# Kernel optimization log

Measured on AMD Instinct MI355X. Metric: run time of the kernel, lower is better.

## Reference

```python
import jax, jax.numpy as jnp
import numpy as np

N_NODES = 100000
N_EDGES = 1600000
IN_F = 512
OUT_F = 128


def setup_inputs() -> dict:
    key = jax.random.key(0)
    k1, k2, k3, k4, k5 = jax.random.split(key, 5)
    x = jax.random.normal(k1, (N_NODES, IN_F), dtype=jnp.float32)
    adj_row = jnp.sort(jax.random.randint(k2, (N_EDGES,), 0, N_NODES, dtype=jnp.int32))
    adj_col = jax.random.randint(k3, (N_EDGES,), 0, N_NODES, dtype=jnp.int32)
    adj_vals = jax.random.uniform(k4, (N_EDGES,), dtype=jnp.float32)
    # Xavier-uniform init like nn.init.xavier_uniform_
    limit = float(np.sqrt(6.0 / (IN_F + OUT_F)))
    weight = jax.random.uniform(k5, (IN_F, OUT_F), minval=-limit, maxval=limit, dtype=jnp.float32)
    return {"x": x, "adj_row": adj_row, "adj_col": adj_col, "adj_vals": adj_vals, "weight": weight}


def reference(x, adj_row, adj_col, adj_vals, weight):
    # support = input @ weight  (dense GEMM; torch.spmm with dense-equivalent input)
    support = x @ weight                      # [N, OUT_F]
    # output = adj @ support, adj in COO: gather cols, scale, segment-sum by row
    msgs = adj_vals[:, None] * support[adj_col]          # [E, OUT_F]
    output = jax.ops.segment_sum(msgs, adj_row, num_segments=N_NODES)  # [N, OUT_F]
    return output
```

## Files before the change

kernel.cpp:

```cpp
#include <hip/hip_runtime.h>
#include <hip/hip_bf16.h>

typedef __bf16 bf16;
typedef __attribute__((ext_vector_type(8))) __bf16 bf16x8;
typedef __attribute__((ext_vector_type(4))) __bf16 bf16x4;
typedef __attribute__((ext_vector_type(2))) __bf16 bf16x2;
typedef __attribute__((ext_vector_type(4))) float f32x4;

#define IN_F 512
#define OUT_F 128
#define BM 64
#define BK 64
#define NKT (IN_F / BK)
#define RPW 8
#define WPB 4
#define PAGE 256
#define UNR 16

__global__ __launch_bounds__(256) void wt_convert_kernel(const float* __restrict__ w,
                                                         bf16* __restrict__ wt_frag) {
    int o = blockIdx.x * 256 + threadIdx.x;
    int e   = o & 7;
    int l   = (o >> 3) & 63;
    int nb  = (o >> 9) & 7;
    int kkt = o >> 12;
    int n = nb * 16 + (l & 15);
    int k = (kkt >> 1) * 64 + (kkt & 1) * 32 + (l >> 4) * 8 + e;
    wt_frag[o] = (bf16)w[k * OUT_F + n];
}

__global__ __launch_bounds__(256) void row_ptr_kernel(const int* __restrict__ adj_row,
                                                      int* __restrict__ row_ptr,
                                                      int n_edges, int n_nodes) {
    int e = blockIdx.x * 256 + threadIdx.x;
    if (e >= n_edges) return;
    int r1 = adj_row[e];
    int r0 = (e == 0) ? -1 : adj_row[e - 1];
    for (int r = r0 + 1; r <= r1; ++r) row_ptr[r] = e;
    if (e == n_edges - 1)
        for (int r = r1 + 1; r <= n_nodes; ++r) row_ptr[r] = n_edges;
}

__global__ __launch_bounds__(256) void gemm_kernel(const float* __restrict__ x,
                                                   const bf16* __restrict__ wt_frag,
                                                   bf16* __restrict__ support,
                                                   int n_nodes) {
    __shared__ bf16 As[2][BM * BK];

    const int tid  = threadIdx.x;
    const int lane = tid & 63;
    const int wid  = tid >> 6;
    const int row0 = blockIdx.x * BM;

    float4 av[4];

    auto load_tile = [&](int kt) {
        const int k0 = kt * BK;
        #pragma unroll
        for (int i = 0; i < 4; ++i) {
            int li = i * 256 + tid;
            int r = li >> 4, c4 = li & 15;
            int grow = row0 + r;
            float4 v = {0.f, 0.f, 0.f, 0.f};
            if (grow < n_nodes)
                v = *reinterpret_cast<const float4*>(x + (size_t)grow * IN_F + k0 + c4 * 4);
            av[i] = v;
        }
    };

    auto write_tile = [&](int buf) {
        char* Ab = (char*)As[buf];
        #pragma unroll
        for (int i = 0; i < 4; ++i) {
            int li = i * 256 + tid;
            int r = li >> 4, c4 = li & 15;
            bf16x4 b;
            b[0] = (bf16)av[i].x; b[1] = (bf16)av[i].y;
            b[2] = (bf16)av[i].z; b[3] = (bf16)av[i].w;
            *reinterpret_cast<bf16x4*>(Ab + ((r * 128 + c4 * 8) ^ ((r & 7) << 4))) = b;
        }
    };

    load_tile(0);
    write_tile(0);
    __syncthreads();

    f32x4 acc[4][2] = {};

    for (int kt = 0; kt < NKT; ++kt) {
        const int cur = kt & 1;

        bf16x8 b[2][2];
        #pragma unroll
        for (int kk = 0; kk < 2; ++kk)
            #pragma unroll
            for (int n = 0; n < 2; ++n) {
                int f = (kt * 2 + kk) * 8 + (wid * 2 + n);
                b[kk][n] = *reinterpret_cast<const bf16x8*>(wt_frag + ((size_t)f * 64 + lane) * 8);
            }

        if (kt < NKT - 1) load_tile(kt + 1);

        const char* Ab = (const char*)As[cur];
        #pragma unroll
        for (int kk = 0; kk < 2; ++kk) {
            const int kbyte = kk * 64 + (lane >> 4) * 16;
            bf16x8 a[4];
            #pragma unroll
            for (int m = 0; m < 4; ++m) {
                int r = m * 16 + (lane & 15);
                a[m] = *reinterpret_cast<const bf16x8*>(Ab + ((r * 128 + kbyte) ^ ((r & 7) << 4)));
            }
            #pragma unroll
            for (int m = 0; m < 4; ++m)
                #pragma unroll
                for (int n = 0; n < 2; ++n)
                    acc[m][n] = __builtin_amdgcn_mfma_f32_16x16x32_bf16(a[m], b[kk][n], acc[m][n], 0, 0, 0);
        }

        if (kt < NKT - 1) {
            write_tile(cur ^ 1);
            __syncthreads();
        }
    }

    #pragma unroll
    for (int m = 0; m < 4; ++m) {
        #pragma unroll
        for (int n = 0; n < 2; ++n) {
            #pragma unroll
            for (int j = 0; j < 4; ++j) {
                int gm = row0 + m * 16 + (lane >> 4) * 4 + j;
                int gn = wid * 32 + n * 16 + (lane & 15);
                if (gm < n_nodes)
                    support[(size_t)gm * OUT_F + gn] = (bf16)acc[m][n][j];
            }
        }
    }
}

__global__ __launch_bounds__(256, 8) void scatter_kernel(const int* __restrict__ adj_row,
                                                         const int* __restrict__ adj_col,
                                                         const float* __restrict__ adj_vals,
                                                         const bf16* __restrict__ support,
                                                         const int* __restrict__ row_ptr,
                                                         float* __restrict__ out,
                                                         int n_nodes) {
    __shared__ int   srow[WPB][PAGE];
    __shared__ int   scol[WPB][PAGE];
    __shared__ float sval[WPB][PAGE];

    const int t  = threadIdx.x & 63;
    const int w  = threadIdx.x >> 6;
    const int r0 = blockIdx.x * (WPB * RPW) + w * RPW;
    if (r0 >= n_nodes) return;
    const int rEnd = min(r0 + RPW, n_nodes);
    const int eLo  = row_ptr[r0];
    const int eHi  = row_ptr[rEnd];

    float accx = 0.f, accy = 0.f;
    int   cur  = r0;

    auto flush_to = [&](int rNew) {
        if (cur < rEnd) {
            float2 st = {accx, accy};
            *reinterpret_cast<float2*>(out + (size_t)cur * OUT_F + t * 2) = st;
        }
        float2 z = {0.f, 0.f};
        int zhi = rNew < rEnd ? rNew : rEnd;
        for (int r = cur + 1; r < zhi; ++r)
            *reinterpret_cast<float2*>(out + (size_t)r * OUT_F + t * 2) = z;
        accx = 0.f; accy = 0.f;
        cur = rNew;
    };

    for (int base = eLo; base < eHi; base += PAGE) {
        const int nE = min(PAGE, eHi - base);
        for (int i = t; i < nE; i += 64) {
            srow[w][i] = adj_row[base + i];
            scol[w][i] = adj_col[base + i];
            sval[w][i] = adj_vals[base + i];
        }
        const int nEpad = (nE + UNR - 1) & ~(UNR - 1);
        {
            int i = nE + t;
            if (i < nEpad) {
                srow[w][i] = n_nodes;
                scol[w][i] = 0;
                sval[w][i] = 0.f;
            }
        }

        for (int i0 = 0; i0 < nE; i0 += UNR) {
            unsigned int u[UNR];
            #pragma unroll
            for (int k = 0; k < UNR; ++k) {
                int c = scol[w][i0 + k];
                u[k] = *reinterpret_cast<const unsigned int*>(support + (size_t)c * OUT_F + t * 2);
            }
            #pragma unroll
            for (int k = 0; k < UNR; ++k) {
                int r = srow[w][i0 + k];
                if (r != cur) flush_to(r);
                float  s = sval[w][i0 + k];
                bf16x2 v = __builtin_bit_cast(bf16x2, u[k]);
                accx += s * (float)v[0];
                accy += s * (float)v[1];
            }
        }
    }
    flush_to(rEnd);
}

extern "C" void kernel_launch(void* const* d_in, const int* in_sizes, int n_in,
                              void* d_out, int out_size, void* d_ws, size_t ws_size,
                              hipStream_t stream) {
    const float* x        = (const float*)d_in[0];
    const int*   adj_row  = (const int*)d_in[1];
    const int*   adj_col  = (const int*)d_in[2];
    const float* adj_vals = (const float*)d_in[3];
    const float* weight   = (const float*)d_in[4];
    float*       out      = (float*)d_out;

    const int n_nodes = in_sizes[0] / IN_F;
    const int n_edges = in_sizes[1];

    char* ws = (char*)d_ws;
    bf16* support = (bf16*)ws;
    bf16* wt_frag = (bf16*)(ws + (size_t)n_nodes * OUT_F * 2);
    int*  row_ptr = (int*)(ws + (size_t)n_nodes * OUT_F * 2 + IN_F * OUT_F * 2);

    wt_convert_kernel<<<(IN_F * OUT_F) / 256, 256, 0, stream>>>(weight, wt_frag);

    row_ptr_kernel<<<(n_edges + 255) / 256, 256, 0, stream>>>(adj_row, row_ptr,
                                                              n_edges, n_nodes);

    int gemm_blocks = (n_nodes + BM - 1) / BM;
    gemm_kernel<<<gemm_blocks, 256, 0, stream>>>(x, wt_frag, support, n_nodes);

    int scat_blocks = (n_nodes + WPB * RPW - 1) / (WPB * RPW);
    scatter_kernel<<<scat_blocks, WPB * 64, 0, stream>>>(adj_row, adj_col, adj_vals,
                                                         support, row_ptr, out, n_nodes);
}
```

Baseline: 123.4 us.

## Deepen GEMM global-load prefetch to three tiles and merge setup kernels

The GEMM now keeps three register sets of x tiles in flight, loading tile kt+3 while computing tile kt, and double-buffers the weight fragments in registers so the next k-step's B is fetched one iteration early. The fully unrolled k-loop lets the compiler index the register arrays statically. Separately, the weight-conversion and row_ptr kernels are fused into one launch to remove a kernel launch. The deeper prefetch raises register pressure (48 extra float4 registers plus B buffers), which may reduce occupancy for the memory-bound GEMM.

```diff
diff --git a/kernel.cpp b/kernel.cpp
--- a/kernel.cpp
+++ b/kernel.cpp
@@ -16,29 +16,31 @@
 #define WPB 4
 #define PAGE 256
 #define UNR 16
-
-__global__ __launch_bounds__(256) void wt_convert_kernel(const float* __restrict__ w,
-                                                         bf16* __restrict__ wt_frag) {
-    int o = blockIdx.x * 256 + threadIdx.x;
-    int e   = o & 7;
-    int l   = (o >> 3) & 63;
-    int nb  = (o >> 9) & 7;
-    int kkt = o >> 12;
-    int n = nb * 16 + (l & 15);
-    int k = (kkt >> 1) * 64 + (kkt & 1) * 32 + (l >> 4) * 8 + e;
-    wt_frag[o] = (bf16)w[k * OUT_F + n];
-}
-
-__global__ __launch_bounds__(256) void row_ptr_kernel(const int* __restrict__ adj_row,
-                                                      int* __restrict__ row_ptr,
-                                                      int n_edges, int n_nodes) {
-    int e = blockIdx.x * 256 + threadIdx.x;
-    if (e >= n_edges) return;
-    int r1 = adj_row[e];
-    int r0 = (e == 0) ? -1 : adj_row[e - 1];
-    for (int r = r0 + 1; r <= r1; ++r) row_ptr[r] = e;
-    if (e == n_edges - 1)
-        for (int r = r1 + 1; r <= n_nodes; ++r) row_ptr[r] = n_edges;
+#define WT_BLOCKS 256
+
+__global__ __launch_bounds__(256) void setup_kernel(const float* __restrict__ w,
+                                                    bf16* __restrict__ wt_frag,
+                                                    const int* __restrict__ adj_row,
+                                                    int* __restrict__ row_ptr,
+                                                    int n_edges, int n_nodes) {
+    if (blockIdx.x < WT_BLOCKS) {
+        int o = blockIdx.x * 256 + threadIdx.x;
+        int e   = o & 7;
+        int l   = (o >> 3) & 63;
+        int nb  = (o >> 9) & 7;
+        int kkt = o >> 12;
+        int n = nb * 16 + (l & 15);
+        int k = (kkt >> 1) * 64 + (kkt & 1) * 32 + (l >> 4) * 8 + e;
+        wt_frag[o] = (bf16)w[k * OUT_F + n];
+    } else {
+        int e = (blockIdx.x - WT_BLOCKS) * 256 + threadIdx.x;
+        if (e >= n_edges) return;
+        int r1 = adj_row[e];
+        int r0 = (e == 0) ? -1 : adj_row[e - 1];
+        for (int r = r0 + 1; r <= r1; ++r) row_ptr[r] = e;
+        if (e == n_edges - 1)
+            for (int r = r1 + 1; r <= n_nodes; ++r) row_ptr[r] = n_edges;
+    }
 }
 
 __global__ __launch_bounds__(256) void gemm_kernel(const float* __restrict__ x,
@@ -52,9 +54,10 @@
     const int wid  = tid >> 6;
     const int row0 = blockIdx.x * BM;
 
-    float4 av[4];
-
-    auto load_tile = [&](int kt) {
+    float4 av[3][4];
+    bf16x8 bfr[2][2][2];
+
+    auto load_tile = [&](int set, int kt) {
         const int k0 = kt * BK;
         #pragma unroll
         for (int i = 0; i < 4; ++i) {
@@ -64,44 +67,48 @@
             float4 v = {0.f, 0.f, 0.f, 0.f};
             if (grow < n_nodes)
                 v = *reinterpret_cast<const float4*>(x + (size_t)grow * IN_F + k0 + c4 * 4);
-            av[i] = v;
-        }
-    };
-
-    auto write_tile = [&](int buf) {
+            av[set][i] = v;
+        }
+    };
+
+    auto load_b = [&](int p, int kt) {
+        #pragma unroll
+        for (int kk = 0; kk < 2; ++kk)
+            #pragma unroll
+            for (int n = 0; n < 2; ++n) {
+                int f = (kt * 2 + kk) * 8 + (wid * 2 + n);
+                bfr[p][kk][n] = *reinterpret_cast<const bf16x8*>(wt_frag + ((size_t)f * 64 + lane) * 8);
+            }
+    };
+
+    auto write_tile = [&](int set, int buf) {
         char* Ab = (char*)As[buf];
         #pragma unroll
         for (int i = 0; i < 4; ++i) {
             int li = i * 256 + tid;
             int r = li >> 4, c4 = li & 15;
             bf16x4 b;
-            b[0] = (bf16)av[i].x; b[1] = (bf16)av[i].y;
-            b[2] = (bf16)av[i].z; b[3] = (bf16)av[i].w;
+            b[0] = (bf16)av[set][i].x; b[1] = (bf16)av[set][i].y;
+            b[2] = (bf16)av[set][i].z; b[3] = (bf16)av[set][i].w;
             *reinterpret_cast<bf16x4*>(Ab + ((r * 128 + c4 * 8) ^ ((r & 7) << 4))) = b;
         }
     };
 
-    load_tile(0);
-    write_tile(0);
+    load_tile(0, 0);
+    write_tile(0, 0);
+    load_tile(1, 1);
+    load_tile(2, 2);
+    load_b(0, 0);
     __syncthreads();
 
     f32x4 acc[4][2] = {};
 
+    #pragma unroll
     for (int kt = 0; kt < NKT; ++kt) {
-        const int cur = kt & 1;
-
-        bf16x8 b[2][2];
-        #pragma unroll
-        for (int kk = 0; kk < 2; ++kk)
-            #pragma unroll
-            for (int n = 0; n < 2; ++n) {
-                int f = (kt * 2 + kk) * 8 + (wid * 2 + n);
-                b[kk][n] = *reinterpret_cast<const bf16x8*>(wt_frag + ((size_t)f * 64 + lane) * 8);
-            }
-
-        if (kt < NKT - 1) load_tile(kt + 1);
-
-        const char* Ab = (const char*)As[cur];
+        if (kt + 1 < NKT) load_b((kt + 1) & 1, kt + 1);
+        if (kt + 3 < NKT) load_tile(kt % 3, kt + 3);
+
+        const char* Ab = (const char*)As[kt & 1];
         #pragma unroll
         for (int kk = 0; kk < 2; ++kk) {
             const int kbyte = kk * 64 + (lane >> 4) * 16;
@@ -115,11 +122,11 @@
             for (int m = 0; m < 4; ++m)
                 #pragma unroll
                 for (int n = 0; n < 2; ++n)
-                    acc[m][n] = __builtin_amdgcn_mfma_f32_16x16x32_bf16(a[m], b[kk][n], acc[m][n], 0, 0, 0);
-        }
-
-        if (kt < NKT - 1) {
-            write_tile(cur ^ 1);
+                    acc[m][n] = __builtin_amdgcn_mfma_f32_16x16x32_bf16(a[m], bfr[kt & 1][kk][n], acc[m][n], 0, 0, 0);
+        }
+
+        if (kt + 1 < NKT) {
+            write_tile((kt + 1) % 3, (kt + 1) & 1);
             __syncthreads();
         }
     }
@@ -230,10 +237,9 @@
     bf16* wt_frag = (bf16*)(ws + (size_t)n_nodes * OUT_F * 2);
     int*  row_ptr = (int*)(ws + (size_t)n_nodes * OUT_F * 2 + IN_F * OUT_F * 2);
 
-    wt_convert_kernel<<<(IN_F * OUT_F) / 256, 256, 0, stream>>>(weight, wt_frag);
-
-    row_ptr_kernel<<<(n_edges + 255) / 256, 256, 0, stream>>>(adj_row, row_ptr,
-                                                              n_edges, n_nodes);
+    int setup_blocks = WT_BLOCKS + (n_edges + 255) / 256;
+    setup_kernel<<<setup_blocks, 256, 0, stream>>>(weight, wt_frag, adj_row,
+                                                   row_ptr, n_edges, n_nodes);
 
     int gemm_blocks = (n_nodes + BM - 1) / BM;
     gemm_kernel<<<gemm_blocks, 256, 0, stream>>>(x, wt_frag, support, n_nodes);
```

Result: no change. 122.4 us (median of 2 runs) (-0.8%).
